# Performance work log

Measured on AMD Instinct MI355X. Metric: run time of the kernel, lower is better.

The kernel has to match this reference:

```python
import jax, jax.numpy as jnp
import numpy as np

B, C_IN, C_OUT, H, W = 4, 256, 256, 64, 64
KH = KW = 3
STRIDE = 1
PAD = 1
DIL = 1


def setup_inputs() -> dict:
    key = jax.random.key(0)
    k1, k2, k3, k4 = jax.random.split(key, 4)
    x = jax.random.normal(k1, (B, C_IN, H, W), dtype=jnp.float32)
    # torchvision layout: 2*dg*KH*KW channels, (y, x) pair per kernel tap
    offset = jax.random.normal(k2, (B, 2 * KH * KW, H, W), dtype=jnp.float32)
    fan_in = C_IN * KH * KW
    weight = jax.random.normal(k3, (C_OUT, C_IN, KH, KW), dtype=jnp.float32) / np.sqrt(fan_in)
    bias = jax.random.normal(k4, (C_OUT,), dtype=jnp.float32) * 0.01
    return {"x": x, "offset": offset, "weight": weight, "bias": bias}


def _gather_bilinear_corner(x_flat, yi, xi, h, w):
    # x_flat: [B, C, H*W]; yi/xi: [B, KK, Ho, Wo] int32
    valid = ((yi >= 0) & (yi < h) & (xi >= 0) & (xi < w)).astype(x_flat.dtype)
    idx = jnp.clip(yi, 0, h - 1) * w + jnp.clip(xi, 0, w - 1)
    b = idx.shape[0]
    g = jnp.take_along_axis(x_flat, idx.reshape(b, 1, -1), axis=2)
    return g.reshape(b, x_flat.shape[1], *yi.shape[1:]), valid


def deform_conv2d(x, offset, weight, bias):
    b, c, h, w = x.shape
    o = weight.shape[0]
    kk = KH * KW
    ho = (h + 2 * PAD - DIL * (KH - 1) - 1) // STRIDE + 1
    wo = (w + 2 * PAD - DIL * (KW - 1) - 1) // STRIDE + 1

    ky = (jnp.arange(kk, dtype=jnp.float32) // KW) * DIL  # [KK]
    kx = (jnp.arange(kk, dtype=jnp.float32) % KW) * DIL
    hs = jnp.arange(ho, dtype=jnp.float32) * STRIDE - PAD   # [Ho]
    ws = jnp.arange(wo, dtype=jnp.float32) * STRIDE - PAD   # [Wo]

    off = offset.reshape(b, kk, 2, ho, wo)
    py = hs[None, None, :, None] + ky[None, :, None, None] + off[:, :, 0]  # [B,KK,Ho,Wo]
    px = ws[None, None, None, :] + kx[None, :, None, None] + off[:, :, 1]

    y0 = jnp.floor(py)
    x0 = jnp.floor(px)
    wy1 = py - y0  # fractional parts, differentiable w.r.t. offsets
    wx1 = px - x0
    wy0 = 1.0 - wy1
    wx0 = 1.0 - wx1
    y0i = y0.astype(jnp.int32)
    x0i = x0.astype(jnp.int32)

    x_flat = x.reshape(b, c, h * w)
    corners = [
        (y0i,     x0i,     wy0 * wx0),
        (y0i,     x0i + 1, wy0 * wx1),
        (y0i + 1, x0i,     wy1 * wx0),
        (y0i + 1, x0i + 1, wy1 * wx1),
    ]
    sampled = jnp.zeros((b, c, kk, ho, wo), dtype=x.dtype)
    for yi, xi, wgt in corners:
        g, valid = _gather_bilinear_corner(x_flat, yi, xi, h, w)
        sampled = sampled + g * (wgt * valid)[:, None]

    out = jnp.einsum('bckhw,ock->bohw', sampled, weight.reshape(o, c, kk))
    return out + bias[None, :, None, None]


def reference(x, offset, weight, bias):
    return deform_conv2d(x, offset, weight, bias)
```

## Files before the change

kernel.cpp:

```cpp
#include <hip/hip_runtime.h>

typedef __bf16 bf16;
typedef __bf16 bf16x4 __attribute__((ext_vector_type(4)));
typedef __bf16 bf16x8 __attribute__((ext_vector_type(8)));
typedef float  f32x4  __attribute__((ext_vector_type(4)));

#define CIN   256
#define KK    9
#define KDIM  2304
#define KITERS 72
#define PXW   32

__device__ __forceinline__ float sread(float f) {
    return __builtin_bit_cast(float,
        __builtin_amdgcn_readfirstlane(__builtin_bit_cast(int, f)));
}
__device__ __forceinline__ int sreadi(int v) {
    return __builtin_amdgcn_readfirstlane(v);
}

__global__ __launch_bounds__(256) void prep_k(const float* __restrict__ x,
                                              const float* __restrict__ w,
                                              bf16* __restrict__ xt,
                                              bf16* __restrict__ wq) {
    int bid = blockIdx.x;
    int tid = threadIdx.x;
    if (bid < 1024) {
        __shared__ bf16 tile[64][72];
        int pt = bid & 63, ct = (bid >> 6) & 3, b = bid >> 8;
        int lane = tid & 63, row = tid >> 6;
        const float* src = x + ((size_t)(b * 256 + ct * 64)) * 4096 + pt * 64;
        #pragma unroll
        for (int cc = row; cc < 64; cc += 4)
            tile[lane][cc] = (bf16)src[(size_t)cc * 4096 + lane];
        __syncthreads();
        bf16* dst = xt + ((size_t)(b * 4096 + pt * 64)) * 256 + ct * 64;
        int p = tid >> 3, j = tid & 7;
        #pragma unroll
        for (int pp = p; pp < 64; pp += 32)
            *reinterpret_cast<bf16x8*>(dst + (size_t)pp * 256 + j * 8) =
                *reinterpret_cast<const bf16x8*>(&tile[pp][j * 8]);
    } else {
        int idx  = (bid - 1024) * 256 + tid;
        int j    = idx & 7;
        int lane = (idx >> 3) & 63;
        int rest = idx >> 9;
        int kt   = rest % KITERS;
        int m    = rest / KITERS;
        int l16  = lane & 15;
        int quad = lane >> 4;
        int o    = m * 16 + l16;
        int k    = kt * 32 + quad * 8 + j;
        int tap  = k >> 8;
        int cc   = k & 255;
        wq[idx] = (bf16)w[(size_t)o * KDIM + cc * KK + tap];
    }
}

__global__ __launch_bounds__(1024, 8) void deform_gemm_k(
    const bf16*  __restrict__ xt,
    const float* __restrict__ off,
    const bf16*  __restrict__ wq,
    const float* __restrict__ bias,
    float*       __restrict__ out) {

    __shared__ bf16 S[2][PXW * 256];

    int tid   = threadIdx.x;
    int wavei = sreadi(tid >> 6);
    int lane  = tid & 63;
    int quad  = lane >> 4;
    int l16   = lane & 15;

    int bid   = blockIdx.x;
    int pb    = ((bid & 7) << 6) | (bid >> 3);
    int pix0  = pb * PXW;
    int b     = pix0 >> 12;
    int pimgb = pix0 & 4095;
    int obase = b * 73728;
    unsigned base = (unsigned)b * 1048576u + (unsigned)(lane * 4);
    int rot   = ((bid >> 3) & 1) * 4;

    f32x4 acc[2];
    acc[0] = (f32x4){0.f, 0.f, 0.f, 0.f};
    acc[1] = (f32x4){0.f, 0.f, 0.f, 0.f};

    for (int t = 0; t < KK; ++t) {
        int tap = t + rot; if (tap >= KK) tap -= KK;
        int ty = tap / 3 - 1;
        int tx = tap % 3 - 1;
        bf16* Sw = &S[t & 1][0];

        #pragma unroll
        for (int i = 0; i < 2; ++i) {
            int n    = wavei * 2 + i;
            int pimg = pimgb + n;
            float oy = off[obase + pimg + (2 * tap) * 4096];
            float ox = off[obase + pimg + (2 * tap + 1) * 4096];
            float py = (float)((pimg >> 6) + ty) + oy;
            float px = (float)((pimg & 63) + tx) + ox;
            float fy = floorf(py), fx = floorf(px);
            int   y0 = (int)fy,    x0 = (int)fx;
            float wy1 = py - fy, wx1 = px - fx;
            float wy0 = 1.f - wy1, wx0 = 1.f - wx1;
            wy0 = ((unsigned)y0       < 64u) ? wy0 : 0.f;
            wy1 = ((unsigned)(y0 + 1) < 64u) ? wy1 : 0.f;
            wx0 = ((unsigned)x0       < 64u) ? wx0 : 0.f;
            wx1 = ((unsigned)(x0 + 1) < 64u) ? wx1 : 0.f;
            int yc0 = min(max(y0, 0), 63), yc1 = min(max(y0 + 1, 0), 63);
            int xc0 = min(max(x0, 0), 63), xc1 = min(max(x0 + 1, 0), 63);
            int u0 = sreadi((yc0 * 64 + xc0) * 256);
            int u1 = sreadi((yc0 * 64 + xc1) * 256);
            int u2 = sreadi((yc1 * 64 + xc0) * 256);
            int u3 = sreadi((yc1 * 64 + xc1) * 256);
            float w0 = sread(wy0 * wx0), w1 = sread(wy0 * wx1);
            float w2 = sread(wy1 * wx0), w3 = sread(wy1 * wx1);
            bf16x4 v0 = *reinterpret_cast<const bf16x4*>(xt + base + (unsigned)u0);
            bf16x4 v1 = *reinterpret_cast<const bf16x4*>(xt + base + (unsigned)u1);
            bf16x4 v2 = *reinterpret_cast<const bf16x4*>(xt + base + (unsigned)u2);
            bf16x4 v3 = *reinterpret_cast<const bf16x4*>(xt + base + (unsigned)u3);
            float a0 = w0 * (float)v0[0] + w1 * (float)v1[0]
                     + w2 * (float)v2[0] + w3 * (float)v3[0];
            float a1 = w0 * (float)v0[1] + w1 * (float)v1[1]
                     + w2 * (float)v2[1] + w3 * (float)v3[1];
            float a2 = w0 * (float)v0[2] + w1 * (float)v1[2]
                     + w2 * (float)v2[2] + w3 * (float)v3[2];
            float a3 = w0 * (float)v0[3] + w1 * (float)v1[3]
                     + w2 * (float)v2[3] + w3 * (float)v3[3];
            bf16x4 sv;
            sv[0] = (bf16)a0; sv[1] = (bf16)a1;
            sv[2] = (bf16)a2; sv[3] = (bf16)a3;
            int gw = lane >> 1;
            int gs = (gw & 24) | ((gw ^ (n & 7)) & 7);
            *reinterpret_cast<bf16x4*>(Sw + n * 256 + gs * 8 + (lane & 1) * 4) = sv;
        }
        __syncthreads();

        const bf16* Sr  = Sw;
        const bf16* ap0 = wq + ((size_t)((wavei * KITERS + tap * 8) * 64 + lane)) * 8;
        #pragma unroll
        for (int kki = 0; kki < 8; ++kki) {
            bf16x8 a = *reinterpret_cast<const bf16x8*>(ap0 + (size_t)kki * 512);
            int g  = kki * 4 + quad;
            int gs = (g & 24) | ((g ^ (l16 & 7)) & 7);
            bf16x8 b0 = *reinterpret_cast<const bf16x8*>(Sr + l16 * 256 + gs * 8);
            bf16x8 b1 = *reinterpret_cast<const bf16x8*>(Sr + (16 + l16) * 256 + gs * 8);
            acc[0] = __builtin_amdgcn_mfma_f32_16x16x32_bf16(a, b0, acc[0], 0, 0, 0);
            acc[1] = __builtin_amdgcn_mfma_f32_16x16x32_bf16(a, b1, acc[1], 0, 0, 0);
        }
    }

    #pragma unroll
    for (int nt = 0; nt < 2; ++nt) {
        int pg   = pix0 + nt * 16 + l16;
        int bb   = pg >> 12;
        int pimg = pg & 4095;
        int m    = wavei * 16 + quad * 4;
        float* op = out + ((size_t)(bb * 256 + m)) * 4096 + pimg;
        #pragma unroll
        for (int r = 0; r < 4; ++r)
            op[(size_t)r * 4096] = acc[nt][r] + bias[m + r];
    }
}

extern "C" void kernel_launch(void* const* d_in, const int* in_sizes, int n_in,
                              void* d_out, int out_size, void* d_ws, size_t ws_size,
                              hipStream_t stream) {
    const float* x    = (const float*)d_in[0];
    const float* off  = (const float*)d_in[1];
    const float* w    = (const float*)d_in[2];
    const float* bias = (const float*)d_in[3];
    float* out = (float*)d_out;

    bf16* wq = (bf16*)d_ws;
    bf16* xt = (bf16*)((char*)d_ws + (size_t)589824 * 2);

    prep_k<<<3328, 256, 0, stream>>>(x, w, xt, wq);
    deform_gemm_k<<<512, 1024, 0, stream>>>(xt, off, wq, bias, out);
}
```

Measured before the change: 116.7 us.

## Switch GEMM to 32x32x16 MFMA with split-K across wave halves and LDS reduction

Each of the 16 waves now computes a 32-out-channel by 32-pixel tile with the 32x32x16 bf16 MFMA. K is split in half between waves 0-7 and 8-15, and the two partial sums are combined through shared memory before the output is written. The weight prepack layout and the LDS swizzle are changed to match the new MFMA operand layout. The first four weight fragments are loaded before the barrier so their latency overlaps the sampling phase. The aim is fewer, larger MFMAs and fewer LDS B-fragment reads per MAC, at the cost of an extra reduction pass with two barriers.

```diff
diff --git a/kernel.cpp b/kernel.cpp
--- a/kernel.cpp
+++ b/kernel.cpp
@@ -3,13 +3,13 @@
 typedef __bf16 bf16;
 typedef __bf16 bf16x4 __attribute__((ext_vector_type(4)));
 typedef __bf16 bf16x8 __attribute__((ext_vector_type(8)));
-typedef float  f32x4  __attribute__((ext_vector_type(4)));
-
-#define CIN   256
-#define KK    9
-#define KDIM  2304
-#define KITERS 72
-#define PXW   32
+typedef float  f32x16 __attribute__((ext_vector_type(16)));
+
+#define CIN    256
+#define KK     9
+#define KDIM   2304
+#define KSTEPS 144
+#define PXW    32
 
 __device__ __forceinline__ float sread(float f) {
     return __builtin_bit_cast(float,
@@ -45,12 +45,10 @@
         int j    = idx & 7;
         int lane = (idx >> 3) & 63;
         int rest = idx >> 9;
-        int kt   = rest % KITERS;
-        int m    = rest / KITERS;
-        int l16  = lane & 15;
-        int quad = lane >> 4;
-        int o    = m * 16 + l16;
-        int k    = kt * 32 + quad * 8 + j;
+        int ks   = rest % KSTEPS;
+        int m    = rest / KSTEPS;
+        int o    = m * 32 + (lane & 31);
+        int k    = ks * 16 + (lane >> 5) * 8 + j;
         int tap  = k >> 8;
         int cc   = k & 255;
         wq[idx] = (bf16)w[(size_t)o * KDIM + cc * KK + tap];
@@ -69,8 +67,10 @@
     int tid   = threadIdx.x;
     int wavei = sreadi(tid >> 6);
     int lane  = tid & 63;
-    int quad  = lane >> 4;
-    int l16   = lane & 15;
+    int l32   = lane & 31;
+    int half  = lane >> 5;
+    int mt    = wavei & 7;
+    int kh    = wavei >> 3;
 
     int bid   = blockIdx.x;
     int pb    = ((bid & 7) << 6) | (bid >> 3);
@@ -81,9 +81,9 @@
     unsigned base = (unsigned)b * 1048576u + (unsigned)(lane * 4);
     int rot   = ((bid >> 3) & 1) * 4;
 
-    f32x4 acc[2];
-    acc[0] = (f32x4){0.f, 0.f, 0.f, 0.f};
-    acc[1] = (f32x4){0.f, 0.f, 0.f, 0.f};
+    f32x16 acc;
+    #pragma unroll
+    for (int r = 0; r < 16; ++r) acc[r] = 0.f;
 
     for (int t = 0; t < KK; ++t) {
         int tap = t + rot; if (tap >= KK) tap -= KK;
@@ -130,36 +130,56 @@
             bf16x4 sv;
             sv[0] = (bf16)a0; sv[1] = (bf16)a1;
             sv[2] = (bf16)a2; sv[3] = (bf16)a3;
-            int gw = lane >> 1;
-            int gs = (gw & 24) | ((gw ^ (n & 7)) & 7);
+            int gs = (lane >> 1) ^ (n & 31);
             *reinterpret_cast<bf16x4*>(Sw + n * 256 + gs * 8 + (lane & 1) * 4) = sv;
         }
+
+        const bf16* ap0 = wq +
+            ((size_t)(((mt * KSTEPS) + tap * 16 + kh * 8) * 64 + lane)) * 8;
+        bf16x8 a0 = *reinterpret_cast<const bf16x8*>(ap0);
+        bf16x8 a1 = *reinterpret_cast<const bf16x8*>(ap0 + 512);
+        bf16x8 a2 = *reinterpret_cast<const bf16x8*>(ap0 + 1024);
+        bf16x8 a3 = *reinterpret_cast<const bf16x8*>(ap0 + 1536);
+
         __syncthreads();
 
-        const bf16* Sr  = Sw;
-        const bf16* ap0 = wq + ((size_t)((wavei * KITERS + tap * 8) * 64 + lane)) * 8;
-        #pragma unroll
-        for (int kki = 0; kki < 8; ++kki) {
-            bf16x8 a = *reinterpret_cast<const bf16x8*>(ap0 + (size_t)kki * 512);
-            int g  = kki * 4 + quad;
-            int gs = (g & 24) | ((g ^ (l16 & 7)) & 7);
-            bf16x8 b0 = *reinterpret_cast<const bf16x8*>(Sr + l16 * 256 + gs * 8);
-            bf16x8 b1 = *reinterpret_cast<const bf16x8*>(Sr + (16 + l16) * 256 + gs * 8);
-            acc[0] = __builtin_amdgcn_mfma_f32_16x16x32_bf16(a, b0, acc[0], 0, 0, 0);
-            acc[1] = __builtin_amdgcn_mfma_f32_16x16x32_bf16(a, b1, acc[1], 0, 0, 0);
+        const bf16* Sr = Sw;
+        #pragma unroll
+        for (int kk2 = 0; kk2 < 8; ++kk2) {
+            bf16x8 a;
+            if      (kk2 == 0) a = a0;
+            else if (kk2 == 1) a = a1;
+            else if (kk2 == 2) a = a2;
+            else if (kk2 == 3) a = a3;
+            else a = *reinterpret_cast<const bf16x8*>(ap0 + (size_t)kk2 * 512);
+            int s  = kh * 8 + kk2;
+            int g  = s * 2 + half;
+            int gs = g ^ l32;
+            bf16x8 bf = *reinterpret_cast<const bf16x8*>(Sr + l32 * 256 + gs * 8);
+            acc = __builtin_amdgcn_mfma_f32_32x32x16_bf16(a, bf, acc, 0, 0, 0);
         }
     }
 
-    #pragma unroll
-    for (int nt = 0; nt < 2; ++nt) {
-        int pg   = pix0 + nt * 16 + l16;
-        int bb   = pg >> 12;
-        int pimg = pg & 4095;
-        int m    = wavei * 16 + quad * 4;
-        float* op = out + ((size_t)(bb * 256 + m)) * 4096 + pimg;
-        #pragma unroll
-        for (int r = 0; r < 4; ++r)
-            op[(size_t)r * 4096] = acc[nt][r] + bias[m + r];
+    __syncthreads();
+    float* Sf = reinterpret_cast<float*>(&S[0][0]);
+    if (wavei >= 8) {
+        int wb = (wavei - 8) * 64 + lane;
+        #pragma unroll
+        for (int r = 0; r < 16; ++r)
+            Sf[r * 512 + wb] = acc[r];
+    }
+    __syncthreads();
+    if (wavei < 8) {
+        int wb   = wavei * 64 + lane;
+        int m    = mt * 32;
+        int pimg = pimgb + l32;
+        float* op = out + ((size_t)(b * 256 + m)) * 4096 + pimg;
+        #pragma unroll
+        for (int r = 0; r < 16; ++r) {
+            int row = (r & 3) + 8 * (r >> 2) + half * 4;
+            float v = acc[r] + Sf[r * 512 + wb] + bias[m + row];
+            op[(size_t)row * 4096] = v;
+        }
     }
 }
 
```

Result: slower. 119.7 us (+2.6%).
